# Kernel optimization log

Measured on AMD Instinct MI355X. Metric: run time of the kernel, lower is better.

The kernel has to match this reference:

```python
import jax, jax.numpy as jnp
import numpy as np

EPS = 1e-5
GROUPS = 16  # 2*channels // chgn = 128 // 8


def _dft(xr, xi, inverse=False):
    """Matmul-based DFT along the last axis. xi may be None (real input)."""
    N = xr.shape[-1]
    n = jnp.arange(N, dtype=xr.dtype)
    ang = (2.0 * np.pi / N) * (n[:, None] * n[None, :])
    c, s = jnp.cos(ang), jnp.sin(ang)
    if xi is None:
        xi = jnp.zeros_like(xr)
    if inverse:
        yr = (xr @ c - xi @ s) / N
        yi = (xi @ c + xr @ s) / N
    else:
        yr = xr @ c + xi @ s
        yi = xi @ c - xr @ s
    return yr, yi


def _rfft(x):
    w = x.shape[-1]
    yr, yi = _dft(x, None, False)                 # DFT along width
    yr, yi = yr[..., : w // 2 + 1], yi[..., : w // 2 + 1]
    yr, yi = jnp.swapaxes(yr, -1, -2), jnp.swapaxes(yi, -1, -2)
    yr, yi = _dft(yr, yi, False)                  # DFT along height
    return jnp.swapaxes(yr, -1, -2), jnp.swapaxes(yi, -1, -2)


def _irfft(xr, xi):
    yr, yi = jnp.swapaxes(xr, -1, -2), jnp.swapaxes(xi, -1, -2)
    yr, yi = _dft(yr, yi, True)                   # inverse DFT along height
    yr, yi = jnp.swapaxes(yr, -1, -2), jnp.swapaxes(yi, -1, -2)
    # hermitian reconstruction along width
    yr = jnp.concatenate([yr, jnp.flip(yr[..., 1:-1], axis=-1)], axis=-1)
    yi = jnp.concatenate([yi, -jnp.flip(yi[..., 1:-1], axis=-1)], axis=-1)
    yr, _ = _dft(yr, yi, True)                    # inverse DFT along width, keep real
    return yr


def _block(y, conv_w, conv_b, gn_gamma, gn_beta):
    # 1x1 conv
    y = jnp.einsum('bchw,oc->bohw', y, conv_w) + conv_b[None, :, None, None]
    B, C, H, W = y.shape
    yg = y.reshape(B, GROUPS, C // GROUPS, H, W)
    mu = yg.mean(axis=(2, 3, 4), keepdims=True)
    var = yg.var(axis=(2, 3, 4), keepdims=True)
    yg = (yg - mu) * jax.lax.rsqrt(var + EPS)
    y = yg.reshape(B, C, H, W) * gn_gamma[None, :, None, None] + gn_beta[None, :, None, None]
    return jax.nn.relu(y)  # dropout=0.0 -> identity


def _fu(x, conv_w, conv_b, gn_gamma, gn_beta):
    ch = x.shape[1]
    yr, yi = _rfft(x)
    y = jnp.concatenate([yr, yi], axis=1)
    y = _block(y, conv_w, conv_b, gn_gamma, gn_beta)
    return _irfft(y[:, :ch], y[:, ch:])


def setup_inputs() -> dict:
    key = jax.random.key(0)
    k1, k2 = jax.random.split(key)
    x = jax.random.normal(k1, (4, 64, 256, 256), dtype=jnp.float32)
    conv_w = jax.random.normal(k2, (128, 128), dtype=jnp.float32) * (1.0 / np.sqrt(128.0))
    conv_b = jnp.zeros((128,), dtype=jnp.float32)
    gn_gamma = jnp.ones((128,), dtype=jnp.float32)
    gn_beta = jnp.zeros((128,), dtype=jnp.float32)
    return {"x": x, "conv_w": conv_w, "conv_b": conv_b, "gn_gamma": gn_gamma, "gn_beta": gn_beta}


def reference(x, conv_w, conv_b, gn_gamma, gn_beta):
    h = x.shape[2]
    bot = _fu(x[:, :, :-1, :], conv_w, conv_b, gn_gamma, gn_beta)
    top = _fu(x[:, :, 1:, :], conv_w, conv_b, gn_gamma, gn_beta)
    return jnp.concatenate([bot[:, :, : h // 2, :], top[:, :, h // 2 - 1 :, :]], axis=2)
```

## Files before the change

### kernel.cpp

```cpp
#include <hip/hip_runtime.h>
#include <math.h>

#define TPB 256

typedef unsigned short us16;
typedef __bf16 bf16x8 __attribute__((ext_vector_type(8)));
typedef float f32x4 __attribute__((ext_vector_type(4)));

static const int B_ALL = 4;
static const int CH   = 64;
static const int HIN  = 256, WIN = 256;
static const int HH   = 255;
static const int WF   = 129;
static const int HWF  = HH * WF;
static const int SP   = WF * 256;
static const int KH   = 160;
static const int UZ   = 64 * WF;
#define GN_EPS 1e-5f

__device__ __forceinline__ us16 f2bf(float f) {
  union { float f; unsigned u; } v; v.f = f;
  unsigned r = v.u + 0x7FFFu + ((v.u >> 16) & 1u);
  return (us16)(r >> 16);
}
__device__ __forceinline__ float bf2f(us16 v) {
  union { unsigned u; float f; } t; t.u = ((unsigned)v) << 16; return t.f;
}
__device__ __forceinline__ void gload16(const void* g, void* l) {
  __builtin_amdgcn_global_load_lds(
      (const __attribute__((address_space(1))) unsigned int*)g,
      (__attribute__((address_space(3))) unsigned int*)l, 16, 0, 0);
}
#define MFMA __builtin_amdgcn_mfma_f32_16x16x32_bf16
#define WAITVM(N) asm volatile("s_waitcnt vmcnt(" #N ")" ::: "memory")
#define BAR_ACQ() do { \
    __builtin_amdgcn_s_barrier(); \
    asm volatile("" ::: "memory"); \
    __builtin_amdgcn_sched_barrier(0); } while (0)
#define BAR_REL() do { \
    asm volatile("" ::: "memory"); \
    __builtin_amdgcn_s_barrier(); } while (0)

__global__ __launch_bounds__(TPB) void k_zero(float* __restrict__ out, int n) {
  int i = blockIdx.x * TPB + threadIdx.x;
  if (i < n) out[i] = 0.f;
}

__global__ __launch_bounds__(TPB) void k_xcast2(const float* __restrict__ x,
                                                us16* __restrict__ xb,
                                                us16* __restrict__ Frt,
                                                us16* __restrict__ Fit) {
  const int row = blockIdx.x * 4 + (threadIdx.x >> 6);
  const int lane = threadIdx.x & 63;
  float4 v = ((const float4*)(x + (size_t)row * 256))[lane];
  ushort4 o;
  o.x = f2bf(v.x); o.y = f2bf(v.y); o.z = f2bf(v.z); o.w = f2bf(v.w);
  ((ushort4*)(xb + (size_t)row * 256))[lane] = o;
  float alt = v.x - v.y + v.z - v.w;
  for (int off = 32; off; off >>= 1) alt += __shfl_down(alt, off);
  if (lane == 0) {
    int bc = row >> 8, h = row & 255;
    size_t idx = ((size_t)bc * WF + 128) * 256 + h;
    Frt[idx] = f2bf(alt);
    Fit[idx] = 0;
  }
}

__global__ __launch_bounds__(TPB) void k_tables(
    us16* __restrict__ CbA, us16* __restrict__ SbA,
    us16* __restrict__ Tcb, us16* __restrict__ Tsb,
    us16* __restrict__ Tci, us16* __restrict__ Tsi,
    us16* __restrict__ Wpb, us16* __restrict__ Wqb,
    const float* __restrict__ conv_w) {
  int i = blockIdx.x * TPB + threadIdx.x;
  const double PI2 = 6.283185307179586476925286766559;
  if (i < 2 * 65536) {
    int fu = i >> 16, r = (i >> 8) & 255, k = i & 255;
    float cv = 0.f, sv = 0.f;
    int kk = k - fu;
    if (r < 255 && kk >= 0 && kk < 255) {
      double ang = PI2 * (double)((r * kk) % 255) / 255.0;
      cv = (float)cos(ang); sv = (float)sin(ang);
    }
    CbA[i] = f2bf(cv); SbA[i] = f2bf(sv);
  }
  if (i < 128 * 256) {
    int n = i >> 8, w = i & 255;
    double ang = PI2 * (double)((n * w) & 255) / 256.0;
    Tcb[i] = f2bf((float)cos(ang));
    Tsb[i] = f2bf((float)sin(ang));
  }
  if (i < 256 * KH) {
    int w = i / KH, k = i - w * KH;
    float cv = 0.f, sv = 0.f;
    if (k < WF) {
      double coef = (k == 0 || k == 128) ? 1.0 : 2.0;
      double ang = PI2 * (double)((k * w) & 255) / 256.0;
      cv = (float)(coef * cos(ang) / 256.0);
      sv = (float)(coef * sin(ang) / 256.0);
    }
    Tci[i] = f2bf(cv); Tsi[i] = f2bf(sv);
  }
  if (i < 128 * 128) {
    int o = i >> 7, c = i & 127;
    Wpb[i] = f2bf(conv_w[i]);
    float q = (c < 64) ? -conv_w[o * 128 + 64 + c] : conv_w[o * 128 + c - 64];
    Wqb[i] = f2bf(q);
  }
}

__global__ __launch_bounds__(TPB) void k_dftw_fwd_mfma(
    const us16* __restrict__ xb, const us16* __restrict__ Tcb,
    const us16* __restrict__ Tsb, us16* __restrict__ Frt, us16* __restrict__ Fit) {
  __shared__ __align__(16) us16 Ac[2][64][32];
  __shared__ __align__(16) us16 As[2][64][32];
  __shared__ __align__(16) us16 Bx[2][64][32];
  const int tid = threadIdx.x, w = tid >> 6, lane = tid & 63;
  const int hb = blockIdx.x;
  const int n0 = blockIdx.y * 64;
  const int rsel = lane >> 2;
  const int csw = (lane & 3) ^ ((lane >> 3) & 3);
  const us16* gAc = Tcb + (size_t)(n0 + 16 * w + rsel) * 256 + csw * 8;
  const us16* gAs = Tsb + (size_t)(n0 + 16 * w + rsel) * 256 + csw * 8;
  const us16* gB  = xb + ((size_t)hb * 64 + 16 * w + rsel) * 256 + csw * 8;
  f32x4 accr[4] = {}, acci[4] = {};
  const int fr = lane & 15;
  const int kb = 8 * ((lane >> 4) ^ ((lane >> 1) & 3));
#define STAGE_K1(pp, k0) do { \
    gload16(gAc + (k0), &Ac[pp][16 * w][0]); \
    gload16(gAs + (k0), &As[pp][16 * w][0]); \
    gload16(gB + (k0), &Bx[pp][16 * w][0]); } while (0)
  STAGE_K1(0, 0);
  int pp = 0;
  for (int k0 = 0; k0 < 256; k0 += 32) {
    if (k0 + 32 < 256) { STAGE_K1(pp ^ 1, k0 + 32); WAITVM(3); }
    else WAITVM(0);
    BAR_ACQ();
    bf16x8 aC = *(const bf16x8*)&Ac[pp][16 * w + fr][kb];
    bf16x8 aS = *(const bf16x8*)&As[pp][16 * w + fr][kb];
    uint4 su = *(const uint4*)&aS;
    su.x ^= 0x80008000u; su.y ^= 0x80008000u; su.z ^= 0x80008000u; su.w ^= 0x80008000u;
    bf16x8 aSn = *(const bf16x8*)&su;
#pragma unroll
    for (int t = 0; t < 4; ++t) {
      bf16x8 b = *(const bf16x8*)&Bx[pp][16 * t + fr][kb];
      accr[t] = MFMA(aC, b, accr[t], 0, 0, 0);
      acci[t] = MFMA(aSn, b, acci[t], 0, 0, 0);
    }
    BAR_REL();
    pp ^= 1;
  }
  const int bc = hb >> 2, hl = (hb & 3) * 64;
#pragma unroll
  for (int t = 0; t < 4; ++t) {
    int h = hl + 16 * t + fr;
#pragma unroll
    for (int j = 0; j < 4; ++j) {
      int n = n0 + 16 * w + 4 * (lane >> 4) + j;
      size_t idx = ((size_t)bc * WF + n) * 256 + h;
      Frt[idx] = f2bf(accr[t][j]);
      Fit[idx] = f2bf(acci[t][j]);
    }
  }
}

__global__ __launch_bounds__(TPB) void k_mix(
    const us16* __restrict__ Frt, const us16* __restrict__ Fit,
    const us16* __restrict__ Wpb, const us16* __restrict__ Wqb,
    us16* __restrict__ P, us16* __restrict__ Q) {
  __shared__ __align__(16) us16 Ap[64][32];
  __shared__ __align__(16) us16 Aq[64][32];
  __shared__ __align__(8)  us16 Bs[64][36];
  const int tid = threadIdx.x, w = tid >> 6, lane = tid & 63;
  const int sp0 = blockIdx.x * 64, o0 = blockIdx.y * 64, b = blockIdx.z;
  const int rsel = lane >> 2;
  const int csw = (lane & 3) ^ ((lane >> 3) & 3);
  const us16* gAp = Wpb + (size_t)(o0 + 16 * w + rsel) * 128 + csw * 8;
  const us16* gAq = Wqb + (size_t)(o0 + 16 * w + rsel) * 128 + csw * 8;
  f32x4 accp[4] = {}, accq[4] = {};
  const int fr = lane & 15;
  const int kbA = 8 * ((lane >> 4) ^ ((lane >> 1) & 3));
  const int kbB = 8 * (lane >> 4);
  for (int c0 = 0; c0 < 128; c0 += 32) {
    gload16(gAp + c0, &Ap[16 * w][0]);
    gload16(gAq + c0, &Aq[16 * w][0]);
    for (int f = tid; f < 1024; f += TPB) {
      int cl = f >> 5, spp = f & 31;
      int c = c0 + cl;
      const us16* src = (c < 64) ? Frt : Fit;
      size_t addr = (size_t)(b * 64 + (c & 63)) * SP + sp0 + 2 * spp;
      unsigned v = *(const unsigned*)(src + addr);
      Bs[2 * spp][cl] = (us16)v;
      Bs[2 * spp + 1][cl] = (us16)(v >> 16);
    }
    __syncthreads();
    bf16x8 aP = *(const bf16x8*)&Ap[16 * w + fr][kbA];
    bf16x8 aQ = *(const bf16x8*)&Aq[16 * w + fr][kbA];
#pragma unroll
    for (int t = 0; t < 4; ++t) {
      uint2 lo = *(const uint2*)&Bs[16 * t + fr][kbB];
      uint2 hi = *(const uint2*)&Bs[16 * t + fr][kbB + 4];
      uint4 qq; qq.x = lo.x; qq.y = lo.y; qq.z = hi.x; qq.w = hi.y;
      bf16x8 bb = *(const bf16x8*)&qq;
      accp[t] = MFMA(aP, bb, accp[t], 0, 0, 0);
      accq[t] = MFMA(aQ, bb, accq[t], 0, 0, 0);
    }
    __syncthreads();
  }
#pragma unroll
  for (int t = 0; t < 4; ++t) {
    int sp = sp0 + 16 * t + fr;
#pragma unroll
    for (int j = 0; j < 4; ++j) {
      int o = o0 + 16 * w + 4 * (lane >> 4) + j;
      size_t idx = (size_t)(b * 128 + o) * SP + sp;
      P[idx] = f2bf(accp[t][j]);
      Q[idx] = f2bf(accq[t][j]);
    }
  }
}

__global__ __launch_bounds__(TPB) void k_dfth_fwd2(
    const us16* __restrict__ P, const us16* __restrict__ Q,
    const us16* __restrict__ CbA, const us16* __restrict__ SbA,
    const float* __restrict__ bias, us16* __restrict__ Yt, int fu) {
  __shared__ __align__(16) us16 Ac[2][2][64][32];
  __shared__ __align__(16) us16 As[2][2][64][32];
  __shared__ __align__(16) us16 Bp[2][64][32];
  __shared__ __align__(16) us16 Bq[2][64][32];
  const int tid = threadIdx.x, w = tid >> 6, lane = tid & 63;
  const int b = blockIdx.z;
  const int u0 = blockIdx.x * 64;
  const int rsel = lane >> 2;
  const int csw = (lane & 3) ^ ((lane >> 3) & 3);
  const us16* gAc = CbA + (((size_t)fu * 256 + 16 * w + rsel) << 8) + csw * 8;
  const us16* gAs = SbA + (((size_t)fu * 256 + 16 * w + rsel) << 8) + csw * 8;
  const us16* gBp = P + (size_t)b * 128 * SP + (size_t)(u0 + 16 * w + rsel) * 256 + csw * 8;
  const us16* gBq = Q + (size_t)b * 128 * SP + (size_t)(u0 + 16 * w + rsel) * 256 + csw * 8;
  f32x4 cp[2][4] = {}, sq[2][4] = {};
  const int fr = lane & 15;
  const int kb = 8 * ((lane >> 4) ^ ((lane >> 1) & 3));
#define STAGE_K3(pp, k0) do { \
    _Pragma("unroll") \
    for (int mt = 0; mt < 2; ++mt) { \
      gload16(gAc + (mt << 14) + (k0), &Ac[pp][mt][16 * w][0]); \
      gload16(gAs + (mt << 14) + (k0), &As[pp][mt][16 * w][0]); } \
    gload16(gBp + (k0), &Bp[pp][16 * w][0]); \
    gload16(gBq + (k0), &Bq[pp][16 * w][0]); } while (0)
  STAGE_K3(0, 0);
  int pp = 0;
  for (int k0 = 0; k0 < 256; k0 += 32) {
    if (k0 + 32 < 256) { STAGE_K3(pp ^ 1, k0 + 32); WAITVM(6); }
    else WAITVM(0);
    BAR_ACQ();
    bf16x8 aC[2], aS[2];
#pragma unroll
    for (int mt = 0; mt < 2; ++mt) {
      aC[mt] = *(const bf16x8*)&Ac[pp][mt][16 * w + fr][kb];
      aS[mt] = *(const bf16x8*)&As[pp][mt][16 * w + fr][kb];
    }
#pragma unroll
    for (int t = 0; t < 4; ++t) {
      bf16x8 bP = *(const bf16x8*)&Bp[pp][16 * t + fr][kb];
      bf16x8 bQ = *(const bf16x8*)&Bq[pp][16 * t + fr][kb];
#pragma unroll
      for (int mt = 0; mt < 2; ++mt) {
        cp[mt][t] = MFMA(aC[mt], bP, cp[mt][t], 0, 0, 0);
        sq[mt][t] = MFMA(aS[mt], bQ, sq[mt][t], 0, 0, 0);
      }
    }
    BAR_REL();
    pp ^= 1;
  }
  us16* yb = Yt + (size_t)b * 128 * SP;
  const int mb_ = 16 * w + 4 * (lane >> 4);
#pragma unroll
  for (int t = 0; t < 4; ++t) {
    int u = u0 + 16 * t + fr;
    float bo = bias[u / WF];
#pragma unroll
    for (int mt = 0; mt < 2; ++mt) {
      int base = mt * 64 + mb_;
      float y[4], z[4];
#pragma unroll
      for (int j = 0; j < 4; ++j) {
        y[j] = cp[mt][t][j] + sq[mt][t][j] + bo;
        z[j] = cp[mt][t][j] - sq[mt][t][j] + bo;
      }
      uint2 pk;
      pk.x = (unsigned)f2bf(y[0]) | ((unsigned)f2bf(y[1]) << 16);
      pk.y = (unsigned)f2bf(y[2]) | ((unsigned)f2bf(y[3]) << 16);
      *(uint2*)(yb + (size_t)u * 256 + base) = pk;
      uint2 pk2;
      pk2.x = (unsigned)f2bf(z[3]) | ((unsigned)f2bf(z[2]) << 16);
      pk2.y = (unsigned)f2bf(z[1]) | ((unsigned)f2bf(z[0]) << 16);
      *(uint2*)(yb + (size_t)u * 256 + 252 - base) = pk2;
    }
  }
}

__global__ __launch_bounds__(TPB) void k_gn_part(const us16* __restrict__ Yt,
                                                 float* __restrict__ part) {
  const int tid = threadIdx.x;
  const int bz = blockIdx.x, b = bz >> 7, ch = bz & 127;
  const us16* p = Yt + (size_t)b * 128 * SP + (size_t)ch * SP;
  float s = 0.f, ss = 0.f;
  for (int cch = tid; cch < 129 * 32; cch += TPB) {
    int n = cch >> 5, off = (cch & 31) * 8;
    uint4 v = *(const uint4*)(p + (size_t)n * 256 + off);
    unsigned q[4] = {v.x, v.y, v.z, v.w};
#pragma unroll
    for (int u = 0; u < 4; ++u) {
      float f0 = __uint_as_float(q[u] << 16);
      float f1 = __uint_as_float(q[u] & 0xffff0000u);
      s += f0 + f1; ss += f0 * f0 + f1 * f1;
    }
    if ((cch & 31) == 31) {
      float f = __uint_as_float(v.w & 0xffff0000u);
      s -= f; ss -= f * f;
    }
  }
  __shared__ float rs[TPB], rq[TPB];
  rs[tid] = s; rq[tid] = ss;
  __syncthreads();
  for (int st = TPB / 2; st > 0; st >>= 1) {
    if (tid < st) { rs[tid] += rs[tid + st]; rq[tid] += rq[tid + st]; }
    __syncthreads();
  }
  if (tid == 0) { part[bz * 2] = rs[0]; part[bz * 2 + 1] = rq[0]; }
}

__global__ void k_gn_stats(const float* __restrict__ part,
                           float* __restrict__ stats, int nbg) {
  int bg = blockIdx.x * blockDim.x + threadIdx.x;
  if (bg < nbg) {
    float s = 0.f, ss = 0.f;
    for (int j = 0; j < 8; ++j) {
      s += part[(bg * 8 + j) * 2];
      ss += part[(bg * 8 + j) * 2 + 1];
    }
    const float inv = 1.f / (8.f * (float)HWF);
    float mean = s * inv;
    float var = ss * inv - mean * mean;
    stats[bg * 2] = mean;
    stats[bg * 2 + 1] = rsqrtf(var + GN_EPS);
  }
}

__global__ __launch_bounds__(TPB) void k_gnfold(
    const us16* __restrict__ Yt, const float* __restrict__ stats,
    const float* __restrict__ gamma, const float* __restrict__ beta,
    us16* __restrict__ Zrp, us16* __restrict__ Zrm,
    us16* __restrict__ Zip, us16* __restrict__ Zim) {
  const int b = blockIdx.y;
  const int up = blockIdx.x * 8 + (threadIdx.x >> 5);
  const int l32 = threadIdx.x & 31;
  const int c = up / WF;
  const int g1 = b * 16 + (c >> 3), g2 = g1 + 8;
  const float sc1 = gamma[c] * stats[g1 * 2 + 1];
  const float sh1 = beta[c] - stats[g1 * 2] * sc1;
  const float sc2 = gamma[64 + c] * stats[g2 * 2 + 1];
  const float sh2 = beta[64 + c] - stats[g2 * 2] * sc2;
  const us16* ybase = Yt + (size_t)b * 128 * SP;
  const us16* yr = ybase + (size_t)up * 256;
  const us16* yi = ybase + (size_t)(64 * WF + up) * 256;
  const int k0 = l32 * 4;
  uint2 ar = *(const uint2*)(yr + k0);
  uint2 mr = *(const uint2*)(yr + 252 - k0);
  uint2 ai = *(const uint2*)(yi + k0);
  uint2 mi = *(const uint2*)(yi + 252 - k0);
  us16 arv[4] = {(us16)ar.x, (us16)(ar.x >> 16), (us16)ar.y, (us16)(ar.y >> 16)};
  us16 mrv[4] = {(us16)mr.x, (us16)(mr.x >> 16), (us16)mr.y, (us16)(mr.y >> 16)};
  us16 aiv[4] = {(us16)ai.x, (us16)(ai.x >> 16), (us16)ai.y, (us16)(ai.y >> 16)};
  us16 miv[4] = {(us16)mi.x, (us16)(mi.x >> 16), (us16)mi.y, (us16)(mi.y >> 16)};
  us16 rp[4], rm[4], ip[4], im[4];
#pragma unroll
  for (int d = 0; d < 4; ++d) {
    float zr = fmaxf(bf2f(arv[d]) * sc1 + sh1, 0.f);
    float zi = fmaxf(bf2f(aiv[d]) * sc2 + sh2, 0.f);
    float pr = 0.f, pi = 0.f;
    if (k0 + d > 0) {
      pr = fmaxf(bf2f(mrv[3 - d]) * sc1 + sh1, 0.f);
      pi = fmaxf(bf2f(miv[3 - d]) * sc2 + sh2, 0.f);
    }
    rp[d] = f2bf(zr + pr); rm[d] = f2bf(zr - pr);
    ip[d] = f2bf(zi + pi); im[d] = f2bf(zi - pi);
  }
  const size_t zo = ((size_t)b * UZ + up) * 128 + k0;
  uint2 o1; o1.x = (unsigned)rp[0] | ((unsigned)rp[1] << 16);
  o1.y = (unsigned)rp[2] | ((unsigned)rp[3] << 16);
  *(uint2*)(Zrp + zo) = o1;
  uint2 o2; o2.x = (unsigned)rm[0] | ((unsigned)rm[1] << 16);
  o2.y = (unsigned)rm[2] | ((unsigned)rm[3] << 16);
  *(uint2*)(Zrm + zo) = o2;
  uint2 o3; o3.x = (unsigned)ip[0] | ((unsigned)ip[1] << 16);
  o3.y = (unsigned)ip[2] | ((unsigned)ip[3] << 16);
  *(uint2*)(Zip + zo) = o3;
  uint2 o4; o4.x = (unsigned)im[0] | ((unsigned)im[1] << 16);
  o4.y = (unsigned)im[2] | ((unsigned)im[3] << 16);
  *(uint2*)(Zim + zo) = o4;
}

__global__ __launch_bounds__(TPB) void k_dfth_inv_mfma(
    const us16* __restrict__ Zrp, const us16* __restrict__ Zrm,
    const us16* __restrict__ Zip, const us16* __restrict__ Zim,
    const us16* __restrict__ CbA, const us16* __restrict__ SbA,
    us16* __restrict__ Hr, us16* __restrict__ Hi, int hsel) {
  __shared__ __align__(16) us16 Ac[2][2][64][32];
  __shared__ __align__(16) us16 As[2][2][64][32];
  __shared__ __align__(16) us16 Brp[2][64][32];
  __shared__ __align__(16) us16 Brm[2][64][32];
  __shared__ __align__(16) us16 Bip[2][64][32];
  __shared__ __align__(16) us16 Bim[2][64][32];
  const int tid = threadIdx.x, w = tid >> 6, lane = tid & 63;
  const int b = blockIdx.z;
  const int u0 = blockIdx.x * 64;
  const int rsel = lane >> 2;
  const int csw = (lane & 3) ^ ((lane >> 3) & 3);
  const us16* gAc = CbA + (((size_t)hsel + 16 * w + rsel) << 8) + csw * 8;
  const us16* gAs = SbA + (((size_t)hsel + 16 * w + rsel) << 8) + csw * 8;
  const size_t zoff = ((size_t)b * UZ + u0 + 16 * w + rsel) * 128 + csw * 8;
  const us16* gZrp = Zrp + zoff;
  const us16* gZrm = Zrm + zoff;
  const us16* gZip = Zip + zoff;
  const us16* gZim = Zim + zoff;
  f32x4 accr[2][4] = {}, acci[2][4] = {};
  const int fr = lane & 15;
  const int kb = 8 * ((lane >> 4) ^ ((lane >> 1) & 3));
#define STAGE_K6(pp, k0) do { \
    gload16(gAc + (k0), &Ac[pp][0][16 * w][0]); \
    gload16(gAc + (1 << 14) + (k0), &Ac[pp][1][16 * w][0]); \
    gload16(gAs + (k0), &As[pp][0][16 * w][0]); \
    gload16(gAs + (1 << 14) + (k0), &As[pp][1][16 * w][0]); \
    gload16(gZrp + (k0), &Brp[pp][16 * w][0]); \
    gload16(gZrm + (k0), &Brm[pp][16 * w][0]); \
    gload16(gZip + (k0), &Bip[pp][16 * w][0]); \
    gload16(gZim + (k0), &Bim[pp][16 * w][0]); } while (0)
  STAGE_K6(0, 0);
  int pp = 0;
  for (int k0 = 0; k0 < 128; k0 += 32) {
    if (k0 + 32 < 128) { STAGE_K6(pp ^ 1, k0 + 32); WAITVM(8); }
    else WAITVM(0);
    BAR_ACQ();
    bf16x8 aC[2], aS[2], aSn[2];
#pragma unroll
    for (int mt = 0; mt < 2; ++mt) {
      aC[mt] = *(const bf16x8*)&Ac[pp][mt][16 * w + fr][kb];
      aS[mt] = *(const bf16x8*)&As[pp][mt][16 * w + fr][kb];
      uint4 su = *(const uint4*)&aS[mt];
      su.x ^= 0x80008000u; su.y ^= 0x80008000u; su.z ^= 0x80008000u; su.w ^= 0x80008000u;
      aSn[mt] = *(const bf16x8*)&su;
    }
#pragma unroll
    for (int t = 0; t < 4; ++t) {
      bf16x8 bRp = *(const bf16x8*)&Brp[pp][16 * t + fr][kb];
      bf16x8 bRm = *(const bf16x8*)&Brm[pp][16 * t + fr][kb];
      bf16x8 bIp = *(const bf16x8*)&Bip[pp][16 * t + fr][kb];
      bf16x8 bIm = *(const bf16x8*)&Bim[pp][16 * t + fr][kb];
#pragma unroll
      for (int mt = 0; mt < 2; ++mt) {
        accr[mt][t] = MFMA(aC[mt], bRp, accr[mt][t], 0, 0, 0);
        accr[mt][t] = MFMA(aSn[mt], bIm, accr[mt][t], 0, 0, 0);
        acci[mt][t] = MFMA(aC[mt], bIp, acci[mt][t], 0, 0, 0);
        acci[mt][t] = MFMA(aS[mt], bRm, acci[mt][t], 0, 0, 0);
      }
    }
    BAR_REL();
    pp ^= 1;
  }
  const float inv = 1.f / 255.f;
#pragma unroll
  for (int t = 0; t < 4; ++t) {
    int u = u0 + 16 * t + fr;
    int c = u / WF, n = u - c * WF;
#pragma unroll
    for (int mt = 0; mt < 2; ++mt) {
#pragma unroll
      for (int j = 0; j < 4; ++j) {
        int m = mt * 64 + 16 * w + 4 * (lane >> 4) + j;
        size_t idx = (((size_t)(b * 64 + c)) * 128 + m) * KH + n;
        Hr[idx] = f2bf(accr[mt][t][j] * inv);
        Hi[idx] = f2bf(acci[mt][t][j] * inv);
      }
    }
  }
}

__global__ __launch_bounds__(TPB) void k_dftw_inv_mfma(
    const us16* __restrict__ Hr, const us16* __restrict__ Hi,
    const us16* __restrict__ Tci, const us16* __restrict__ Tsi,
    float* __restrict__ out, int roff, int b0) {
  __shared__ __align__(16) us16 Ar[2][64][32];
  __shared__ __align__(16) us16 Ai[2][64][32];
  __shared__ __align__(16) us16 Bc[2][64][32];
  __shared__ __align__(16) us16 Bs[2][64][32];
  const int tid = threadIdx.x, w = tid >> 6, lane = tid & 63;
  const int w0 = blockIdx.x * 64, mf0 = blockIdx.y * 64;
  const int rsel = lane >> 2;
  const int csw = (lane & 3) ^ ((lane >> 3) & 3);
  const us16* gAr = Hr + (size_t)(mf0 + 16 * w + rsel) * KH + csw * 8;
  const us16* gAi = Hi + (size_t)(mf0 + 16 * w + rsel) * KH + csw * 8;
  const us16* gBc = Tci + (size_t)(w0 + 16 * w + rsel) * KH + csw * 8;
  const us16* gBs = Tsi + (size_t)(w0 + 16 * w + rsel) * KH + csw * 8;
  f32x4 accU[4] = {}, accV[4] = {};
  const int fr = lane & 15;
  const int kb = 8 * ((lane >> 4) ^ ((lane >> 1) & 3));
#define STAGE_K7(pp, k0) do { \
    gload16(gAr + (k0), &Ar[pp][16 * w][0]); \
    gload16(gAi + (k0), &Ai[pp][16 * w][0]); \
    gload16(gBc + (k0), &Bc[pp][16 * w][0]); \
    gload16(gBs + (k0), &Bs[pp][16 * w][0]); } while (0)
  STAGE_K7(0, 0);
  int pp = 0;
  for (int k0 = 0; k0 < KH; k0 += 32) {
    if (k0 + 32 < KH) { STAGE_K7(pp ^ 1, k0 + 32); WAITVM(4); }
    else WAITVM(0);
    BAR_ACQ();
    bf16x8 aR = *(const bf16x8*)&Ar[pp][16 * w + fr][kb];
    bf16x8 aI = *(const bf16x8*)&Ai[pp][16 * w + fr][kb];
    uint4 su = *(const uint4*)&aI;
    su.x ^= 0x80008000u; su.y ^= 0x80008000u; su.z ^= 0x80008000u; su.w ^= 0x80008000u;
    bf16x8 aIn = *(const bf16x8*)&su;
#pragma unroll
    for (int t = 0; t < 4; ++t) {
      bf16x8 bC = *(const bf16x8*)&Bc[pp][16 * t + fr][kb];
      bf16x8 bS = *(const bf16x8*)&Bs[pp][16 * t + fr][kb];
      accU[t] = MFMA(aR, bC, accU[t], 0, 0, 0);
      accV[t] = MFMA(aIn, bS, accV[t], 0, 0, 0);
    }
    BAR_REL();
    pp ^= 1;
  }
#pragma unroll
  for (int t = 0; t < 4; ++t) {
    int wv = w0 + 16 * t + fr;
#pragma unroll
    for (int j = 0; j < 4; ++j) {
      int mf = mf0 + 16 * w + 4 * (lane >> 4) + j;
      int bcl = mf >> 7, mrow = mf & 127;
      int bb = b0 + (bcl >> 6), cc = bcl & 63;
      size_t obase = (((size_t)bb * CH + cc) * HIN + roff + mrow) * WIN;
      float U = accU[t][j], V = accV[t][j];
      out[obase + wv] = U + V;
      if (wv > 0) out[obase + 256 - wv] = U - V;
    }
  }
}

__global__ __launch_bounds__(TPB) void k_w128(const us16* __restrict__ Hr,
                                              float* __restrict__ out,
                                              int roff, int b0) {
  const int mf = blockIdx.x * TPB + threadIdx.x;
  const us16* hr = Hr + (size_t)mf * KH;
  float s = bf2f(hr[0]) + bf2f(hr[128]);
  for (int k = 1; k < 128; k += 2)
    s += -2.f * bf2f(hr[k]) + 2.f * bf2f(hr[k + 1]);
  s -= 2.f * bf2f(hr[128]);
  s *= (1.f / 256.f);
  int bcl = mf >> 7, mrow = mf & 127;
  int bb = b0 + (bcl >> 6), cc = bcl & 63;
  out[(((size_t)bb * CH + cc) * HIN + roff + mrow) * WIN + 128] = s;
}

extern "C" void kernel_launch(void* const* d_in, const int* in_sizes, int n_in,
                              void* d_out, int out_size, void* d_ws, size_t ws_size,
                              hipStream_t stream) {
  const float* x        = (const float*)d_in[0];
  const float* conv_w   = (const float*)d_in[1];
  const float* conv_b   = (const float*)d_in[2];
  const float* gn_gamma = (const float*)d_in[3];
  const float* gn_beta  = (const float*)d_in[4];
  float* out = (float*)d_out;

  const size_t uCbA = 2 * 65536;
  const size_t uTcb = 128 * 256;
  const size_t uTci = (size_t)256 * KH;
  const size_t uW   = 128 * 128;
  const size_t fixed_u16 = 2 * uCbA + 2 * uTcb + 2 * uTci + 2 * uW;
  const size_t uXB = (size_t)CH * HIN * WIN;
  const size_t uF  = (size_t)CH * SP;
  const size_t uPQ = (size_t)128 * SP;
  const size_t uYT = (size_t)128 * SP;
  const size_t uH  = (size_t)CH * 128 * KH;
  const size_t uZ1 = (size_t)UZ * 128;
  const size_t per_u16 = uXB + 2 * uF + 2 * uPQ + 4 * uZ1;

  int nb = 0;
  for (int cand = 4; cand >= 1; cand >>= 1) {
    size_t need = fixed_u16 * 2 + 1152 * 4 + (size_t)cand * per_u16 * 2 + 256;
    if (need <= ws_size) { nb = cand; break; }
  }
  if (nb == 0) {
    k_zero<<<dim3((out_size + TPB - 1) / TPB), dim3(TPB), 0, stream>>>(out, out_size);
    return;
  }

  us16* CbA = (us16*)d_ws;
  us16* SbA = CbA + uCbA;
  us16* Tcb = SbA + uCbA;
  us16* Tsb = Tcb + uTcb;
  us16* Tci = Tsb + uTcb;
  us16* Tsi = Tci + uTci;
  us16* Wpb = Tsi + uTci;
  us16* Wqb = Wpb + uW;
  float* part  = (float*)(Wqb + uW);
  float* stats = part + 1024;
  us16* xb  = (us16*)(stats + 128);
  us16* Frt = xb + (size_t)nb * uXB;
  us16* Fit = Frt + (size_t)nb * uF;
  us16* P   = Fit + (size_t)nb * uF;
  us16* Q   = P + (size_t)nb * uPQ;
  us16* Zrp = Q + (size_t)nb * uPQ;
  us16* Zrm = Zrp + (size_t)nb * uZ1;
  us16* Zip = Zrm + (size_t)nb * uZ1;
  us16* Zim = Zip + (size_t)nb * uZ1;
  us16* Yt  = xb;
  us16* Hr  = xb + (size_t)nb * uYT;
  us16* Hi  = Hr + (size_t)nb * uH;

  k_tables<<<dim3(512), dim3(TPB), 0, stream>>>(CbA, SbA, Tcb, Tsb, Tci, Tsi,
                                                Wpb, Wqb, conv_w);

  for (int b0 = 0; b0 < B_ALL; b0 += nb) {
    k_xcast2<<<dim3(nb * 4096), dim3(TPB), 0, stream>>>(
        x + (size_t)b0 * CH * HIN * WIN, xb, Frt, Fit);
    k_dftw_fwd_mfma<<<dim3(nb * 256, 2), dim3(TPB), 0, stream>>>(
        xb, Tcb, Tsb, Frt, Fit);
    k_mix<<<dim3(SP / 64, 2, nb), dim3(TPB), 0, stream>>>(
        Frt, Fit, Wpb, Wqb, P, Q);
    for (int fu = 0; fu < 2; ++fu) {
      const int hsel = fu ? 127 : 0;
      const int roff = fu ? 128 : 0;
      k_dfth_fwd2<<<dim3(128 * WF / 64, 1, nb), dim3(TPB), 0, stream>>>(
          P, Q, CbA, SbA, conv_b, Yt, fu);
      k_gn_part<<<dim3(nb * 128), dim3(TPB), 0, stream>>>(Yt, part);
      k_gn_stats<<<dim3(1), dim3(64), 0, stream>>>(part, stats, nb * 16);
      k_gnfold<<<dim3(UZ / 8, nb), dim3(TPB), 0, stream>>>(
          Yt, stats, gn_gamma, gn_beta, Zrp, Zrm, Zip, Zim);
      k_dfth_inv_mfma<<<dim3(UZ / 64, 1, nb), dim3(TPB), 0, stream>>>(
          Zrp, Zrm, Zip, Zim, CbA, SbA, Hr, Hi, hsel);
      k_dftw_inv_mfma<<<dim3(2, nb * 128), dim3(TPB), 0, stream>>>(
          Hr, Hi, Tci, Tsi, out, roff, b0);
      k_w128<<<dim3(nb * 32), dim3(TPB), 0, stream>>>(Hr, out, roff, b0);
    }
  }
}
```

Baseline: 267.3 us.

## Fuse GroupNorm partial sums into height-DFT epilogue and widen mix tile

Computes GroupNorm sum and sum-of-squares in the epilogue of the forward height DFT kernel, split per block into two channel segments. This removes the separate k_gn_part pass that re-read Yt, and a new stats kernel reduces the per-block partials by channel group. Separately, k_mix now computes all 128 output channels per block, so each block loads its B tile once instead of twice. The costs are an extra block reduction in shared memory and higher register pressure in k_mix.

```diff
diff --git a/kernel.cpp b/kernel.cpp
--- a/kernel.cpp
+++ b/kernel.cpp
@@ -16,6 +16,7 @@
 static const int SP   = WF * 256;
 static const int KH   = 160;
 static const int UZ   = 64 * WF;
+static const int NBX  = 258;
 #define GN_EPS 1e-5f
 
 __device__ __forceinline__ us16 f2bf(float f) {
@@ -168,22 +169,24 @@
     const us16* __restrict__ Frt, const us16* __restrict__ Fit,
     const us16* __restrict__ Wpb, const us16* __restrict__ Wqb,
     us16* __restrict__ P, us16* __restrict__ Q) {
-  __shared__ __align__(16) us16 Ap[64][32];
-  __shared__ __align__(16) us16 Aq[64][32];
+  __shared__ __align__(16) us16 Ap[2][64][32];
+  __shared__ __align__(16) us16 Aq[2][64][32];
   __shared__ __align__(8)  us16 Bs[64][36];
   const int tid = threadIdx.x, w = tid >> 6, lane = tid & 63;
-  const int sp0 = blockIdx.x * 64, o0 = blockIdx.y * 64, b = blockIdx.z;
+  const int sp0 = blockIdx.x * 64, b = blockIdx.z;
   const int rsel = lane >> 2;
   const int csw = (lane & 3) ^ ((lane >> 3) & 3);
-  const us16* gAp = Wpb + (size_t)(o0 + 16 * w + rsel) * 128 + csw * 8;
-  const us16* gAq = Wqb + (size_t)(o0 + 16 * w + rsel) * 128 + csw * 8;
-  f32x4 accp[4] = {}, accq[4] = {};
+  const us16* gAp0 = Wpb + (size_t)(16 * w + rsel) * 128 + csw * 8;
+  const us16* gAq0 = Wqb + (size_t)(16 * w + rsel) * 128 + csw * 8;
+  f32x4 accp[2][4] = {}, accq[2][4] = {};
   const int fr = lane & 15;
   const int kbA = 8 * ((lane >> 4) ^ ((lane >> 1) & 3));
   const int kbB = 8 * (lane >> 4);
   for (int c0 = 0; c0 < 128; c0 += 32) {
-    gload16(gAp + c0, &Ap[16 * w][0]);
-    gload16(gAq + c0, &Aq[16 * w][0]);
+    gload16(gAp0 + c0, &Ap[0][16 * w][0]);
+    gload16(gAp0 + 64 * 128 + c0, &Ap[1][16 * w][0]);
+    gload16(gAq0 + c0, &Aq[0][16 * w][0]);
+    gload16(gAq0 + 64 * 128 + c0, &Aq[1][16 * w][0]);
     for (int f = tid; f < 1024; f += TPB) {
       int cl = f >> 5, spp = f & 31;
       int c = c0 + cl;
@@ -194,16 +197,20 @@
       Bs[2 * spp + 1][cl] = (us16)(v >> 16);
     }
     __syncthreads();
-    bf16x8 aP = *(const bf16x8*)&Ap[16 * w + fr][kbA];
-    bf16x8 aQ = *(const bf16x8*)&Aq[16 * w + fr][kbA];
+    bf16x8 aP0 = *(const bf16x8*)&Ap[0][16 * w + fr][kbA];
+    bf16x8 aP1 = *(const bf16x8*)&Ap[1][16 * w + fr][kbA];
+    bf16x8 aQ0 = *(const bf16x8*)&Aq[0][16 * w + fr][kbA];
+    bf16x8 aQ1 = *(const bf16x8*)&Aq[1][16 * w + fr][kbA];
 #pragma unroll
     for (int t = 0; t < 4; ++t) {
       uint2 lo = *(const uint2*)&Bs[16 * t + fr][kbB];
       uint2 hi = *(const uint2*)&Bs[16 * t + fr][kbB + 4];
       uint4 qq; qq.x = lo.x; qq.y = lo.y; qq.z = hi.x; qq.w = hi.y;
       bf16x8 bb = *(const bf16x8*)&qq;
-      accp[t] = MFMA(aP, bb, accp[t], 0, 0, 0);
-      accq[t] = MFMA(aQ, bb, accq[t], 0, 0, 0);
+      accp[0][t] = MFMA(aP0, bb, accp[0][t], 0, 0, 0);
+      accp[1][t] = MFMA(aP1, bb, accp[1][t], 0, 0, 0);
+      accq[0][t] = MFMA(aQ0, bb, accq[0][t], 0, 0, 0);
+      accq[1][t] = MFMA(aQ1, bb, accq[1][t], 0, 0, 0);
     }
     __syncthreads();
   }
@@ -211,23 +218,27 @@
   for (int t = 0; t < 4; ++t) {
     int sp = sp0 + 16 * t + fr;
 #pragma unroll
-    for (int j = 0; j < 4; ++j) {
-      int o = o0 + 16 * w + 4 * (lane >> 4) + j;
-      size_t idx = (size_t)(b * 128 + o) * SP + sp;
-      P[idx] = f2bf(accp[t][j]);
-      Q[idx] = f2bf(accq[t][j]);
-    }
+    for (int ot = 0; ot < 2; ++ot)
+#pragma unroll
+      for (int j = 0; j < 4; ++j) {
+        int o = ot * 64 + 16 * w + 4 * (lane >> 4) + j;
+        size_t idx = (size_t)(b * 128 + o) * SP + sp;
+        P[idx] = f2bf(accp[ot][t][j]);
+        Q[idx] = f2bf(accq[ot][t][j]);
+      }
   }
 }
 
 __global__ __launch_bounds__(TPB) void k_dfth_fwd2(
     const us16* __restrict__ P, const us16* __restrict__ Q,
     const us16* __restrict__ CbA, const us16* __restrict__ SbA,
-    const float* __restrict__ bias, us16* __restrict__ Yt, int fu) {
+    const float* __restrict__ bias, us16* __restrict__ Yt,
+    float* __restrict__ gnpart, int fu) {
   __shared__ __align__(16) us16 Ac[2][2][64][32];
   __shared__ __align__(16) us16 As[2][2][64][32];
   __shared__ __align__(16) us16 Bp[2][64][32];
   __shared__ __align__(16) us16 Bq[2][64][32];
+  __shared__ float red[4 * TPB];
   const int tid = threadIdx.x, w = tid >> 6, lane = tid & 63;
   const int b = blockIdx.z;
   const int u0 = blockIdx.x * 64;
@@ -274,10 +285,13 @@
   }
   us16* yb = Yt + (size_t)b * 128 * SP;
   const int mb_ = 16 * w + 4 * (lane >> 4);
+  const int ub = (u0 / WF + 1) * WF;
+  float s0 = 0.f, q0 = 0.f, s1 = 0.f, q1 = 0.f;
 #pragma unroll
   for (int t = 0; t < 4; ++t) {
     int u = u0 + 16 * t + fr;
     float bo = bias[u / WF];
+    float ts = 0.f, tq = 0.f;
 #pragma unroll
     for (int mt = 0; mt < 2; ++mt) {
       int base = mt * 64 + mb_;
@@ -286,6 +300,8 @@
       for (int j = 0; j < 4; ++j) {
         y[j] = cp[mt][t][j] + sq[mt][t][j] + bo;
         z[j] = cp[mt][t][j] - sq[mt][t][j] + bo;
+        ts += y[j]; tq += y[j] * y[j];
+        if (base + j) { ts += z[j]; tq += z[j] * z[j]; }
       }
       uint2 pk;
       pk.x = (unsigned)f2bf(y[0]) | ((unsigned)f2bf(y[1]) << 16);
@@ -296,54 +312,47 @@
       pk2.y = (unsigned)f2bf(z[1]) | ((unsigned)f2bf(z[0]) << 16);
       *(uint2*)(yb + (size_t)u * 256 + 252 - base) = pk2;
     }
-  }
-}
-
-__global__ __launch_bounds__(TPB) void k_gn_part(const us16* __restrict__ Yt,
-                                                 float* __restrict__ part) {
-  const int tid = threadIdx.x;
-  const int bz = blockIdx.x, b = bz >> 7, ch = bz & 127;
-  const us16* p = Yt + (size_t)b * 128 * SP + (size_t)ch * SP;
-  float s = 0.f, ss = 0.f;
-  for (int cch = tid; cch < 129 * 32; cch += TPB) {
-    int n = cch >> 5, off = (cch & 31) * 8;
-    uint4 v = *(const uint4*)(p + (size_t)n * 256 + off);
-    unsigned q[4] = {v.x, v.y, v.z, v.w};
-#pragma unroll
-    for (int u = 0; u < 4; ++u) {
-      float f0 = __uint_as_float(q[u] << 16);
-      float f1 = __uint_as_float(q[u] & 0xffff0000u);
-      s += f0 + f1; ss += f0 * f0 + f1 * f1;
-    }
-    if ((cch & 31) == 31) {
-      float f = __uint_as_float(v.w & 0xffff0000u);
-      s -= f; ss -= f * f;
-    }
-  }
-  __shared__ float rs[TPB], rq[TPB];
-  rs[tid] = s; rq[tid] = ss;
+    if (u >= ub) { s1 += ts; q1 += tq; } else { s0 += ts; q0 += tq; }
+  }
+  __syncthreads();
+  red[tid] = s0; red[TPB + tid] = q0;
+  red[2 * TPB + tid] = s1; red[3 * TPB + tid] = q1;
   __syncthreads();
   for (int st = TPB / 2; st > 0; st >>= 1) {
-    if (tid < st) { rs[tid] += rs[tid + st]; rq[tid] += rq[tid + st]; }
+    if (tid < st) {
+      red[tid] += red[tid + st];
+      red[TPB + tid] += red[TPB + tid + st];
+      red[2 * TPB + tid] += red[2 * TPB + tid + st];
+      red[3 * TPB + tid] += red[3 * TPB + tid + st];
+    }
     __syncthreads();
   }
-  if (tid == 0) { part[bz * 2] = rs[0]; part[bz * 2 + 1] = rq[0]; }
-}
-
-__global__ void k_gn_stats(const float* __restrict__ part,
-                           float* __restrict__ stats, int nbg) {
-  int bg = blockIdx.x * blockDim.x + threadIdx.x;
-  if (bg < nbg) {
+  if (tid == 0) {
+    float* gp = gnpart + ((size_t)b * NBX + blockIdx.x) * 4;
+    gp[0] = red[0]; gp[1] = red[TPB];
+    gp[2] = red[2 * TPB]; gp[3] = red[3 * TPB];
+  }
+}
+
+__global__ void k_gn_stats2(const float* __restrict__ part,
+                            float* __restrict__ stats, int nb) {
+  int i = threadIdx.x;
+  int b = i >> 4, g = i & 15;
+  if (b < nb) {
     float s = 0.f, ss = 0.f;
-    for (int j = 0; j < 8; ++j) {
-      s += part[(bg * 8 + j) * 2];
-      ss += part[(bg * 8 + j) * 2 + 1];
+    const int clo = g * 8, chi = clo + 8;
+    for (int bx = 0; bx < NBX; ++bx) {
+      int c0 = (bx * 64) / WF;
+      int c1 = (bx * 64 + 63) / WF;
+      const float* p = part + ((size_t)b * NBX + bx) * 4;
+      if (c0 >= clo && c0 < chi) { s += p[0]; ss += p[1]; }
+      if (c1 != c0 && c1 >= clo && c1 < chi) { s += p[2]; ss += p[3]; }
     }
     const float inv = 1.f / (8.f * (float)HWF);
     float mean = s * inv;
     float var = ss * inv - mean * mean;
-    stats[bg * 2] = mean;
-    stats[bg * 2 + 1] = rsqrtf(var + GN_EPS);
+    stats[(b * 16 + g) * 2] = mean;
+    stats[(b * 16 + g) * 2 + 1] = rsqrtf(var + GN_EPS);
   }
 }
 
@@ -584,10 +593,11 @@
   const size_t uH  = (size_t)CH * 128 * KH;
   const size_t uZ1 = (size_t)UZ * 128;
   const size_t per_u16 = uXB + 2 * uF + 2 * uPQ + 4 * uZ1;
+  const size_t nPart = 4 * 4 * NBX + 128;
 
   int nb = 0;
   for (int cand = 4; cand >= 1; cand >>= 1) {
-    size_t need = fixed_u16 * 2 + 1152 * 4 + (size_t)cand * per_u16 * 2 + 256;
+    size_t need = fixed_u16 * 2 + nPart * 4 + (size_t)cand * per_u16 * 2 + 256;
     if (need <= ws_size) { nb = cand; break; }
   }
   if (nb == 0) {
@@ -604,7 +614,7 @@
   us16* Wpb = Tsi + uTci;
   us16* Wqb = Wpb + uW;
   float* part  = (float*)(Wqb + uW);
-  float* stats = part + 1024;
+  float* stats = part + 4 * NBX * 4;
   us16* xb  = (us16*)(stats + 128);
   us16* Frt = xb + (size_t)nb * uXB;
   us16* Fit = Frt + (size_t)nb * uF;
@@ -626,15 +636,14 @@
         x + (size_t)b0 * CH * HIN * WIN, xb, Frt, Fit);
     k_dftw_fwd_mfma<<<dim3(nb * 256, 2), dim3(TPB), 0, stream>>>(
         xb, Tcb, Tsb, Frt, Fit);
-    k_mix<<<dim3(SP / 64, 2, nb), dim3(TPB), 0, stream>>>(
+    k_mix<<<dim3(SP / 64, 1, nb), dim3(TPB), 0, stream>>>(
         Frt, Fit, Wpb, Wqb, P, Q);
     for (int fu = 0; fu < 2; ++fu) {
       const int hsel = fu ? 127 : 0;
       const int roff = fu ? 128 : 0;
-      k_dfth_fwd2<<<dim3(128 * WF / 64, 1, nb), dim3(TPB), 0, stream>>>(
-          P, Q, CbA, SbA, conv_b, Yt, fu);
-      k_gn_part<<<dim3(nb * 128), dim3(TPB), 0, stream>>>(Yt, part);
-      k_gn_stats<<<dim3(1), dim3(64), 0, stream>>>(part, stats, nb * 16);
+      k_dfth_fwd2<<<dim3(NBX, 1, nb), dim3(TPB), 0, stream>>>(
+          P, Q, CbA, SbA, conv_b, Yt, part, fu);
+      k_gn_stats2<<<dim3(1), dim3(64), 0, stream>>>(part, stats, nb);
       k_gnfold<<<dim3(UZ / 8, nb), dim3(TPB), 0, stream>>>(
           Yt, stats, gn_gamma, gn_beta, Zrp, Zrm, Zip, Zim);
       k_dfth_inv_mfma<<<dim3(UZ / 64, 1, nb), dim3(TPB), 0, stream>>>(
```

New measurement: 374.0 us. 1.4x slower.
